# Optimization experiments

Measured on AMD Instinct MI355X. Metric: run time of the kernel, lower is better.

Reference implementation:

```python
import jax, jax.numpy as jnp
import numpy as np

B, CIN, H, W = 32, 512, 64, 64
HID, A, C = 256, 9, 20
M = 65536


def setup_inputs() -> dict:
    key = jax.random.key(0)
    k = jax.random.split(key, 7)
    N = B * A * H * W
    features = jax.random.normal(k[0], (B, CIN, H, W), jnp.float32)
    W1 = jax.random.normal(k[1], (HID, CIN), jnp.float32) * 0.02
    b1 = jnp.zeros((HID,), jnp.float32)
    W2 = jax.random.normal(k[2], (5 * A + C, HID), jnp.float32) * 0.02
    b2 = jnp.zeros((5 * A + C,), jnp.float32)
    pos_anchor_idx = jax.random.randint(k[3], (M,), 0, N, jnp.int64 if jax.config.read('jax_enable_x64') else jnp.int32)
    neg_anchor_idx = jax.random.randint(k[4], (M,), 0, N, jnp.int64 if jax.config.read('jax_enable_x64') else jnp.int32)
    return {"features": features, "W1": W1, "b1": b1, "W2": W2, "b2": b2,
            "pos_anchor_idx": pos_anchor_idx, "neg_anchor_idx": neg_anchor_idx}


def reference(features, W1, b1, W2, b2, pos_anchor_idx, neg_anchor_idx):
    Bb, Cin, Hh, Ww = features.shape
    # 1x1 convs are channel GEMMs
    h = jnp.einsum('bchw,oc->bohw', features, W1) + b1[None, :, None, None]
    h = jax.nn.leaky_relu(h, 0.01)  # Dropout2d identity at inference
    out = jnp.einsum('bchw,oc->bohw', h, W2) + b2[None, :, None, None]
    class_scores = out[:, 5 * A:, :, :]                      # (B, C, H, W)
    anchor = out[:, :5 * A, :, :].reshape(Bb, A, 5, Hh, Ww)   # (B, A, 5, H, W)
    conf = jax.nn.sigmoid(anchor[:, :, 0:1])                  # (B, A, 1, H, W)
    off = anchor[:, :, 1:]                                    # (B, A, 4, H, W)
    off = jnp.concatenate([jax.nn.sigmoid(off[:, :, :2]) - 0.5, off[:, :, 2:]], axis=2)
    # extraction: flat layout is b*A*H*W + a*H*W + h*W + w (permute 0,1,3,4,2)
    off_flat = off.transpose(0, 1, 3, 4, 2).reshape(-1, 4)
    conf_flat = conf.transpose(0, 1, 3, 4, 2).reshape(-1, 1)
    offsets = off_flat[pos_anchor_idx]                        # (M, 4)
    conf_out = jnp.concatenate([conf_flat[pos_anchor_idx], conf_flat[neg_anchor_idx]], axis=0)  # (2M, 1)
    # class scores: expand over A is a pure broadcast, so index by (b, spatial) directly
    b_idx = pos_anchor_idx // (A * Hh * Ww)
    sp = pos_anchor_idx % (Hh * Ww)
    cls_flat = class_scores.transpose(0, 2, 3, 1).reshape(Bb * Hh * Ww, -1)
    class_out = cls_flat[b_idx * (Hh * Ww) + sp]              # (M, C)
    return conf_out, offsets, class_out
```

## Files before the change

### kernel.cpp

```cpp
#include <hip/hip_runtime.h>
#include <hip/hip_bf16.h>

typedef __attribute__((ext_vector_type(8)))  __bf16 bf16x8;
typedef __attribute__((ext_vector_type(4)))  __bf16 bf16x4;
typedef __attribute__((ext_vector_type(16))) float  f32x16;
typedef __attribute__((ext_vector_type(4)))  float  f32x4;

#define B_    32
#define CIN   512
#define HID   256
#define HW    4096
#define NA    9
#define NCH   65
#define NPADC 96
#define BN    128
#define M_    65536
#define NTOT  (B_*NA*HW)


static __device__ __forceinline__ float sigf(float v) {
    return 1.f / (1.f + __expf(-v));
}

__global__ void prep_weights(const float* __restrict__ W1, const float* __restrict__ W2,
                             unsigned short* __restrict__ W1bt, unsigned short* __restrict__ W2p) {
    int i = blockIdx.x * 256 + threadIdx.x;
    if (i < 16*256*32) {
        int kt = i >> 13, o = (i >> 5) & 255, kk = i & 31;
        __bf16 h = (__bf16)W1[o*CIN + kt*32 + kk];
        W1bt[i] = __builtin_bit_cast(unsigned short, h);
    } else {
        int j = i - 16*256*32;
        if (j < NPADC*HID) {
            int o = j >> 8, c = j & 255;
            float v = (o < NCH) ? W2[o*HID + c] : 0.f;
            __bf16 h = (__bf16)v;
            W2p[j] = __builtin_bit_cast(unsigned short, h);
        }
    }
}

__launch_bounds__(256, 2)
__global__ void fused_mlp(const float* __restrict__ feat,
                          const float* __restrict__ b1,
                          const float* __restrict__ b2,
                          const unsigned short* __restrict__ W1bt,
                          const unsigned short* __restrict__ W2p,
                          float* __restrict__ conf_d,
                          float* __restrict__ off_d,
                          float* __restrict__ cls_d) {
    __shared__ __align__(16) unsigned char smem[65536];
    unsigned short* As = (unsigned short*)smem;
    unsigned short* Bs = (unsigned short*)(smem + 20480);

    const int tid  = threadIdx.x;
    const int w    = tid >> 6;
    const int lane = tid & 63;
    const int lr   = lane & 31;
    const int lh   = lane >> 5;
    const int bidx = blockIdx.x >> 5;
    const int hw0  = (blockIdx.x & 31) * BN;

    const float* fb = feat + (size_t)bidx * CIN * HW + hw0;

    const int sA  = tid;
    const int sB  = tid & 127;
    const int kgB = tid >> 7;

    f32x16 acc[2][4];
#pragma unroll
    for (int m = 0; m < 2; ++m)
#pragma unroll
        for (int n = 0; n < 4; ++n) acc[m][n] = (f32x16)0.f;

    bf16x8 pa[4];
    float  pb[16];

    auto loadA = [&](int kt) {
        const bf16x8* p = (const bf16x8*)(W1bt + kt*8192 + sA*32);
#pragma unroll
        for (int i = 0; i < 4; ++i) pa[i] = p[i];
    };
    auto loadB = [&](int kt) {
#pragma unroll
        for (int q = 0; q < 2; ++q) {
            int kg = kgB + 2*q;
            const float* src = fb + (size_t)(kt*32 + kg*8) * HW + sB;
#pragma unroll
            for (int j = 0; j < 8; ++j) pb[q*8 + j] = src[(size_t)j * HW];
        }
    };
    auto storeAB = [&]() {
#pragma unroll
        for (int i = 0; i < 4; ++i) *(bf16x8*)(As + sA*40 + i*8) = pa[i];
#pragma unroll
        for (int q = 0; q < 2; ++q) {
            int kg = kgB + 2*q;
            bf16x8 v8;
#pragma unroll
            for (int j = 0; j < 8; ++j) v8[j] = (__bf16)pb[q*8 + j];
            *(bf16x8*)(Bs + sB*40 + kg*8) = v8;
        }
    };

    loadA(0); loadB(0);
    for (int kt = 0; kt < 16; ++kt) {
        storeAB();
        __syncthreads();
        if (kt < 15) { loadA(kt + 1); loadB(kt + 1); }
#pragma unroll
        for (int kk = 0; kk < 2; ++kk) {
            bf16x8 a0 = *(const bf16x8*)(As + (64*w      + lr)*40 + kk*16 + lh*8);
            bf16x8 a1 = *(const bf16x8*)(As + (64*w + 32 + lr)*40 + kk*16 + lh*8);
#pragma unroll
            for (int n = 0; n < 4; ++n) {
                bf16x8 bv = *(const bf16x8*)(Bs + (32*n + lr)*40 + kk*16 + lh*8);
                acc[0][n] = __builtin_amdgcn_mfma_f32_32x32x16_bf16(a0, bv, acc[0][n], 0, 0, 0);
                acc[1][n] = __builtin_amdgcn_mfma_f32_32x32x16_bf16(a1, bv, acc[1][n], 0, 0, 0);
            }
        }
        __syncthreads();
    }

#pragma unroll
    for (int m = 0; m < 2; ++m)
#pragma unroll
        for (int n = 0; n < 4; ++n) {
            int col = 32*n + lr;
            unsigned cswz = (unsigned)((col & 7) << 4);
#pragma unroll
            for (int g = 0; g < 4; ++g) {
                int rbase = 64*w + 32*m + 8*g + 4*lh;
                f32x4 b1v = *(const f32x4*)(b1 + rbase);
                bf16x4 pk;
#pragma unroll
                for (int r = 0; r < 4; ++r) {
                    float v = acc[m][n][4*g + r] + b1v[r];
                    v = v > 0.f ? v : 0.01f * v;
                    pk[r] = (__bf16)v;
                }
                unsigned addr = (unsigned)(col*512 + rbase*2) ^ cswz;
                *(bf16x4*)(smem + addr) = pk;
            }
        }
    __syncthreads();

    f32x16 acc2[3];
#pragma unroll
    for (int m = 0; m < 3; ++m) acc2[m] = (f32x16)0.f;
    const int col2 = 32*w + lr;
    const unsigned cswz2 = (unsigned)((col2 & 7) << 4);
    for (int kt2 = 0; kt2 < 8; ++kt2) {
#pragma unroll
        for (int kk = 0; kk < 2; ++kk) {
            int k0 = kt2*32 + kk*16 + lh*8;
            bf16x8 bv = *(const bf16x8*)(smem + ((unsigned)(col2*512 + k0*2) ^ cswz2));
#pragma unroll
            for (int m = 0; m < 3; ++m) {
                bf16x8 av = *(const bf16x8*)(W2p + (32*m + lr)*256 + k0);
                acc2[m] = __builtin_amdgcn_mfma_f32_32x32x16_bf16(av, bv, acc2[m], 0, 0, 0);
            }
        }
    }

    const int hw     = hw0 + col2;
    const int b9     = bidx * NA;
    const int posIdx = (bidx << 12) + hw;
#pragma unroll
    for (int m = 0; m < 3; ++m)
#pragma unroll
        for (int g = 0; g < 4; ++g) {
            int rbase = 32*m + 8*g + 4*lh;
#pragma unroll
            for (int r = 0; r < 4; ++r) {
                int row = rbase + r;
                if (row >= NCH) continue;
                float v = acc2[m][4*g + r] + b2[row];
                if (row < 45) {
                    int a = row / 5;
                    int j = row - a*5;
                    int abase = ((b9 + a) << 12) + hw;
                    if (j == 0)      conf_d[abase] = sigf(v);
                    else if (j <= 2) off_d[(j-1)*NTOT + abase] = sigf(v) - 0.5f;
                    else             off_d[(j-1)*NTOT + abase] = v;
                } else {
                    cls_d[posIdx*20 + (row - 45)] = v;
                }
            }
        }
}

__global__ void gather_k(const int* __restrict__ pos, const int* __restrict__ neg,
                         const float* __restrict__ conf_d, const float* __restrict__ off_d,
                         const float* __restrict__ cls_d, float* __restrict__ out) {
    int i = blockIdx.x * 256 + threadIdx.x;
    if (i >= M_) return;
    int p = pos[i], q = neg[i];
    out[i]      = conf_d[p];
    out[M_ + i] = conf_d[q];
    f32x4 o;
    o[0] = off_d[p];
    o[1] = off_d[NTOT + p];
    o[2] = off_d[2*NTOT + p];
    o[3] = off_d[3*NTOT + p];
    *(f32x4*)(out + 2*M_ + 4*i) = o;
    int hw = p & 4095;
    int ba = p >> 12;
    int b  = ba / 9;
    const f32x4* c4 = (const f32x4*)(cls_d + (size_t)(b*4096 + hw) * 20);
    f32x4* o4 = (f32x4*)(out + 6*M_ + 20*i);
#pragma unroll
    for (int t = 0; t < 5; ++t) o4[t] = c4[t];
}

extern "C" void kernel_launch(void* const* d_in, const int* in_sizes, int n_in,
                              void* d_out, int out_size, void* d_ws, size_t ws_size,
                              hipStream_t stream) {
    const float* feat = (const float*)d_in[0];
    const float* W1   = (const float*)d_in[1];
    const float* b1   = (const float*)d_in[2];
    const float* W2   = (const float*)d_in[3];
    const float* b2   = (const float*)d_in[4];
    const int*   pos  = (const int*)d_in[5];
    const int*   neg  = (const int*)d_in[6];
    float* out = (float*)d_out;

    char* ws = (char*)d_ws;
    unsigned short* W1bt = (unsigned short*)ws;
    unsigned short* W2p  = (unsigned short*)(ws + 262144);
    float* conf_d = (float*)(ws + 311296);
    float* off_d  = (float*)(ws + 5029888);
    float* cls_d  = (float*)(ws + 23904256);

    prep_weights<<<608, 256, 0, stream>>>(W1, W2, W1bt, W2p);
    fused_mlp<<<1024, 256, 0, stream>>>(feat, b1, b2, W1bt, W2p, conf_d, off_d, cls_d);
    gather_k<<<256, 256, 0, stream>>>(pos, neg, conf_d, off_d, cls_d, out);
}
```

Measured before the change: 108.9 us.

## Stage head outputs through LDS and store offsets/classes as packed bf16

```diff
diff --git a/kernel.cpp b/kernel.cpp
--- a/kernel.cpp
+++ b/kernel.cpp
@@ -47,8 +47,8 @@
                           const unsigned short* __restrict__ W1bt,
                           const unsigned short* __restrict__ W2p,
                           float* __restrict__ conf_d,
-                          float* __restrict__ off_d,
-                          float* __restrict__ cls_d) {
+                          unsigned short* __restrict__ off_w,
+                          unsigned short* __restrict__ cls_w) {
     __shared__ __align__(16) unsigned char smem[65536];
     unsigned short* As = (unsigned short*)smem;
     unsigned short* Bs = (unsigned short*)(smem + 20480);
@@ -163,54 +163,99 @@
         }
     }
 
-    const int hw     = hw0 + col2;
-    const int b9     = bidx * NA;
-    const int posIdx = (bidx << 12) + hw;
+    __syncthreads();
+    float* so = (float*)smem;
 #pragma unroll
     for (int m = 0; m < 3; ++m)
 #pragma unroll
         for (int g = 0; g < 4; ++g) {
             int rbase = 32*m + 8*g + 4*lh;
-#pragma unroll
-            for (int r = 0; r < 4; ++r) {
-                int row = rbase + r;
-                if (row >= NCH) continue;
-                float v = acc2[m][4*g + r] + b2[row];
-                if (row < 45) {
-                    int a = row / 5;
-                    int j = row - a*5;
-                    int abase = ((b9 + a) << 12) + hw;
-                    if (j == 0)      conf_d[abase] = sigf(v);
-                    else if (j <= 2) off_d[(j-1)*NTOT + abase] = sigf(v) - 0.5f;
-                    else             off_d[(j-1)*NTOT + abase] = v;
-                } else {
-                    cls_d[posIdx*20 + (row - 45)] = v;
+            if (rbase <= 64) {
+#pragma unroll
+                for (int r = 0; r < 4; ++r) {
+                    int row = rbase + r;
+                    if (row < NCH) so[row*128 + col2] = acc2[m][4*g + r] + b2[row];
                 }
             }
         }
-}
-
-__global__ void gather_k(const int* __restrict__ pos, const int* __restrict__ neg,
-                         const float* __restrict__ conf_d, const float* __restrict__ off_d,
-                         const float* __restrict__ cls_d, float* __restrict__ out) {
-    int i = blockIdx.x * 256 + threadIdx.x;
-    if (i >= M_) return;
-    int p = pos[i], q = neg[i];
-    out[i]      = conf_d[p];
-    out[M_ + i] = conf_d[q];
-    f32x4 o;
-    o[0] = off_d[p];
-    o[1] = off_d[NTOT + p];
-    o[2] = off_d[2*NTOT + p];
-    o[3] = off_d[3*NTOT + p];
-    *(f32x4*)(out + 2*M_ + 4*i) = o;
-    int hw = p & 4095;
-    int ba = p >> 12;
-    int b  = ba / 9;
-    const f32x4* c4 = (const f32x4*)(cls_d + (size_t)(b*4096 + hw) * 20);
-    f32x4* o4 = (f32x4*)(out + 6*M_ + 20*i);
-#pragma unroll
-    for (int t = 0; t < 5; ++t) o4[t] = c4[t];
+    __syncthreads();
+
+    {
+        const int p   = tid & 127;
+        const int phw = hw0 + p;
+        const int b9  = bidx * NA;
+        if (tid < 128) {
+#pragma unroll
+            for (int a = 0; a < 9; ++a) {
+                float v0 = so[(5*a+0)*128 + p];
+                float v1 = so[(5*a+1)*128 + p];
+                float v2 = so[(5*a+2)*128 + p];
+                float v3 = so[(5*a+3)*128 + p];
+                float v4 = so[(5*a+4)*128 + p];
+                int abase = ((b9 + a) << 12) + phw;
+                conf_d[abase] = sigf(v0);
+                bf16x4 o;
+                o[0] = (__bf16)(sigf(v1) - 0.5f);
+                o[1] = (__bf16)(sigf(v2) - 0.5f);
+                o[2] = (__bf16)v3;
+                o[3] = (__bf16)v4;
+                *(bf16x4*)(off_w + ((size_t)abase << 2)) = o;
+            }
+        } else {
+            unsigned short* dst = cls_w + ((size_t)((bidx << 12) + phw) << 5);
+#pragma unroll
+            for (int q = 0; q < 4; ++q) {
+                bf16x8 v;
+#pragma unroll
+                for (int r = 0; r < 8; ++r) {
+                    int c = q*8 + r;
+                    v[r] = (c < 20) ? (__bf16)so[(45 + c)*128 + p] : (__bf16)0.f;
+                }
+                *(bf16x8*)(dst + q*8) = v;
+            }
+        }
+    }
+}
+
+__global__ void gather_all(const int* __restrict__ pos, const int* __restrict__ neg,
+                           const float* __restrict__ conf_d,
+                           const unsigned short* __restrict__ off_w,
+                           const unsigned short* __restrict__ cls_w,
+                           float* __restrict__ out) {
+    int t = blockIdx.x * 256 + threadIdx.x;
+    if (t < 2*M_) {
+        int idx = (t < M_) ? pos[t] : neg[t - M_];
+        out[t] = conf_d[idx];
+    } else if (t < 3*M_) {
+        int i = t - 2*M_;
+        int p = pos[i];
+        bf16x4 o = *(const bf16x4*)(off_w + ((size_t)p << 2));
+        f32x4 f;
+        f[0] = (float)o[0]; f[1] = (float)o[1];
+        f[2] = (float)o[2]; f[3] = (float)o[3];
+        *(f32x4*)(out + 2*(size_t)M_ + 4*(size_t)i) = f;
+    } else {
+        int i = t - 3*M_;
+        int p = pos[i];
+        int hw = p & 4095;
+        int b  = (p >> 12) / 9;
+        const unsigned short* src = cls_w + ((size_t)((b << 12) + hw) << 5);
+        float* dst = out + 6*(size_t)M_ + 20*(size_t)i;
+        bf16x8 v0 = *(const bf16x8*)(src);
+        bf16x8 v1 = *(const bf16x8*)(src + 8);
+        bf16x4 v2 = *(const bf16x4*)(src + 16);
+        f32x4 f;
+        f[0] = (float)v0[0]; f[1] = (float)v0[1]; f[2] = (float)v0[2]; f[3] = (float)v0[3];
+        *(f32x4*)(dst) = f;
+        f[0] = (float)v0[4]; f[1] = (float)v0[5]; f[2] = (float)v0[6]; f[3] = (float)v0[7];
+        *(f32x4*)(dst + 4) = f;
+        f[0] = (float)v1[0]; f[1] = (float)v1[1]; f[2] = (float)v1[2]; f[3] = (float)v1[3];
+        *(f32x4*)(dst + 8) = f;
+        f[0] = (float)v1[4]; f[1] = (float)v1[5]; f[2] = (float)v1[6]; f[3] = (float)v1[7];
+        *(f32x4*)(dst + 12) = f;
+        f[0] = (float)v2[0]; f[1] = (float)v2[1]; f[2] = (float)v2[2]; f[3] = (float)v2[3];
+        *(f32x4*)(dst + 16) = f;
+    }
 }
 
 extern "C" void kernel_launch(void* const* d_in, const int* in_sizes, int n_in,
@@ -228,11 +273,11 @@
     char* ws = (char*)d_ws;
     unsigned short* W1bt = (unsigned short*)ws;
     unsigned short* W2p  = (unsigned short*)(ws + 262144);
-    float* conf_d = (float*)(ws + 311296);
-    float* off_d  = (float*)(ws + 5029888);
-    float* cls_d  = (float*)(ws + 23904256);
+    float*          conf_d = (float*)(ws + 311296);
+    unsigned short* off_w  = (unsigned short*)(ws + 5029888);
+    unsigned short* cls_w  = (unsigned short*)(ws + 14467072);
 
     prep_weights<<<608, 256, 0, stream>>>(W1, W2, W1bt, W2p);
-    fused_mlp<<<1024, 256, 0, stream>>>(feat, b1, b2, W1bt, W2p, conf_d, off_d, cls_d);
-    gather_k<<<256, 256, 0, stream>>>(pos, neg, conf_d, off_d, cls_d, out);
-}
+    fused_mlp<<<1024, 256, 0, stream>>>(feat, b1, b2, W1bt, W2p, conf_d, off_w, cls_w);
+    gather_all<<<1024, 256, 0, stream>>>(pos, neg, conf_d, off_w, cls_w, out);
+}
```

After: 96.05 us. -11.8%, faster.
